# Performance work log

Hardware: AMD Instinct MI355X
Metric: run time of the kernel (lower is better)

The kernel has to match this reference:

```python
import jax, jax.numpy as jnp
import numpy as np

N = 8192
IN_F = 128
N_HID = 64
OUT_F = 128
NEG = -9.0e15


def _xavier(key, shape, gain=1.414):
    fan_in, fan_out = shape
    a = gain * np.sqrt(6.0 / (fan_in + fan_out))
    return jax.random.uniform(key, shape, jnp.float32, -a, a)


def setup_inputs() -> dict:
    key = jax.random.key(0)
    k_h, k_adj, k_ws, k_wt, k_wc = jax.random.split(key, 5)
    h = jax.random.normal(k_h, (N, IN_F), dtype=jnp.float32)
    adj = jax.random.randint(k_adj, (N, N), 0, 2, dtype=jnp.int32)
    Ws = _xavier(k_ws, (IN_F, N_HID))
    Wt = _xavier(k_wt, (IN_F, N_HID))
    Wc = _xavier(k_wc, (IN_F, OUT_F))
    return {"h": h, "adj": adj, "Ws": Ws, "Wt": Wt, "Wc": Wc}


def reference(h, adj, Ws, Wt, Wc):
    # Whs: [N, H], Wht: [N, H]
    Whs = h @ Ws
    Wht = h @ Wt
    # e: [N, N] dense attention scores
    e = jnp.einsum("nh,mh->nm", Whs, Wht)
    z = jnp.where(adj > 0, e, jnp.asarray(NEG, e.dtype))
    alpha = jax.nn.softmax(z, axis=-1)  # [N, N]
    Whc = h @ Wc                        # [N, OUT_F]
    h_prime = alpha @ Whc               # [N, OUT_F]
    return h_prime
```

## Files before the change

### kernel.cpp

```cpp
#include <hip/hip_runtime.h>


#define NN 8192
#define INF_ 128
#define NHID 64
#define OUTF 128
#define NEGC -9.0e15f

typedef unsigned short u16;
typedef __attribute__((ext_vector_type(8))) short bf16x8;
typedef __attribute__((ext_vector_type(4))) float f32x4;
typedef __attribute__((ext_vector_type(4))) int i32x4;
typedef __attribute__((ext_vector_type(4))) unsigned u32x4;

static __device__ __forceinline__ u16 f2bf(float x) {
  union { float f; unsigned u; } v; v.f = x;
  unsigned lsb = (v.u >> 16) & 1u;
  v.u += 0x7fffu + lsb;
  return (u16)(v.u >> 16);
}
static __device__ __forceinline__ float bf2f(u16 h) {
  union { float f; unsigned u; } v; v.u = ((unsigned)h) << 16;
  return v.f;
}
static __device__ __forceinline__ f32x4 mfma16(bf16x8 a, bf16x8 b, f32x4 c) {
  return __builtin_amdgcn_mfma_f32_16x16x32_bf16(a, b, c, 0, 0, 0);
}

__global__ __launch_bounds__(256) void proj_kernel(
    const float* __restrict__ h, const float* __restrict__ Ws,
    const float* __restrict__ Wt, const float* __restrict__ Wc,
    u16* __restrict__ whs_hi, u16* __restrict__ whs_lo,
    u16* __restrict__ wht_hi, u16* __restrict__ wht_lo,
    u16* __restrict__ whcT) {
  __shared__ f32x4 hbuf[8][32];
  const int tid = threadIdx.x;
  const int r0 = blockIdx.x * 8;
  hbuf[tid >> 5][tid & 31] =
      reinterpret_cast<const f32x4*>(h)[(size_t)r0 * 32 + tid];
  __syncthreads();

  float acc[8];
#pragma unroll
  for (int r = 0; r < 8; ++r) acc[r] = 0.f;

  if (tid < 128) {
    const float* W = (tid < 64) ? (Ws + tid) : (Wt + (tid - 64));
#pragma unroll 4
    for (int k4 = 0; k4 < 32; ++k4) {
      float w0 = W[(k4 * 4 + 0) * NHID];
      float w1 = W[(k4 * 4 + 1) * NHID];
      float w2 = W[(k4 * 4 + 2) * NHID];
      float w3 = W[(k4 * 4 + 3) * NHID];
#pragma unroll
      for (int r = 0; r < 8; ++r) {
        f32x4 hv = hbuf[r][k4];
        acc[r] += hv.x * w0 + hv.y * w1 + hv.z * w2 + hv.w * w3;
      }
    }
    const int col = tid & 63;
    u16* hi = (tid < 64) ? whs_hi : wht_hi;
    u16* lo = (tid < 64) ? whs_lo : wht_lo;
#pragma unroll
    for (int r = 0; r < 8; ++r) {
      float v = acc[r];
      u16 hb = f2bf(v);
      hi[(size_t)(r0 + r) * NHID + col] = hb;
      lo[(size_t)(r0 + r) * NHID + col] = f2bf(v - bf2f(hb));
    }
  } else {
    const int col = tid - 128;
    const float* W = Wc + col;
#pragma unroll 4
    for (int k4 = 0; k4 < 32; ++k4) {
      float w0 = W[(k4 * 4 + 0) * OUTF];
      float w1 = W[(k4 * 4 + 1) * OUTF];
      float w2 = W[(k4 * 4 + 2) * OUTF];
      float w3 = W[(k4 * 4 + 3) * OUTF];
#pragma unroll
      for (int r = 0; r < 8; ++r) {
        f32x4 hv = hbuf[r][k4];
        acc[r] += hv.x * w0 + hv.y * w1 + hv.z * w2 + hv.w * w3;
      }
    }
    union { u16 s[8]; u32x4 v; } pk;
#pragma unroll
    for (int r = 0; r < 8; ++r) pk.s[r] = f2bf(acc[r]);
    *reinterpret_cast<u32x4*>(whcT + (size_t)col * NN + r0) = pk.v;
  }
}

__global__ __launch_bounds__(256, 2) void attn_kernel(
    const u16* __restrict__ whs_hi, const u16* __restrict__ whs_lo,
    const u16* __restrict__ wht_hi, const u16* __restrict__ wht_lo,
    const u16* __restrict__ whcT, const int* __restrict__ adj,
    float* __restrict__ Opart, float* __restrict__ mpart,
    float* __restrict__ lpart, float* __restrict__ out,
    int iters, int cshift, int final_write) {
  __shared__ __align__(16) u16 Bst[2][2][64 * 72];
  __shared__ __align__(16) u16 Wst[2][128 * 64];
  __shared__ __align__(16) u16 Pbuf[4][16][72];
  __shared__ __align__(16) u16 Mbuf[2][64][4];

  const int tid = threadIdx.x;
  const int w = tid >> 6;
  const int lane = tid & 63;
  const int q = lane >> 4;
  const int ln = lane & 15;
  const int chunk = blockIdx.x & ((1 << cshift) - 1);
  const int rb = blockIdx.x >> cshift;
  const int rowB = rb * 64;
  const int row0 = rowB + w * 16;

  const int bcol = tid >> 2;
  const int bsh = (tid >> 1) & 1;
  const int bkh = tid & 1;
  const u16* bg = (bsh ? wht_lo : wht_hi) + (size_t)bcol * NHID + bkh * 32;
  const int wocol = tid >> 1;
  const int wjh = tid & 1;
  const u16* wg = whcT + (size_t)wocol * NN + wjh * 32;
  const int wsw0 = ((2 * wjh + 0) ^ (wocol & 3)) * 16;
  const int wsw1 = ((2 * wjh + 1) ^ (wocol & 3)) * 16;
  const int arow = tid >> 2;
  const int agrp = tid & 3;
  const int* ag = adj + (size_t)(rowB + arow) * NN + agrp * 16;

  bf16x8 a_hi[2], a_lo[2];
#pragma unroll
  for (int kh = 0; kh < 2; ++kh) {
    a_hi[kh] = *reinterpret_cast<const bf16x8*>(
        whs_hi + (size_t)(row0 + ln) * NHID + kh * 32 + q * 8);
    a_lo[kh] = *reinterpret_cast<const bf16x8*>(
        whs_lo + (size_t)(row0 + ln) * NHID + kh * 32 + q * 8);
  }

  f32x4 oacc[8];
#pragma unroll
  for (int ot = 0; ot < 8; ++ot)
#pragma unroll
    for (int g = 0; g < 4; ++g) oacc[ot][g] = 0.f;

  float m_old[4], l_run[4];
#pragma unroll
  for (int g = 0; g < 4; ++g) { m_old[g] = -__builtin_inff(); l_run[g] = 0.f; }

  const int jbase = chunk * iters;

  {
    const size_t j0 = (size_t)jbase * 64;
    const u32x4* p = reinterpret_cast<const u32x4*>(bg + j0 * NHID);
    u32x4 b0 = p[0], b1 = p[1], b2 = p[2], b3 = p[3];
    const u32x4* pw = reinterpret_cast<const u32x4*>(wg + j0);
    u32x4 w0 = pw[0], w1 = pw[1], w2 = pw[2], w3 = pw[3];
    const i32x4* pa = reinterpret_cast<const i32x4*>(ag + j0);
    i32x4 a0 = __builtin_nontemporal_load(pa + 0);
    i32x4 a1 = __builtin_nontemporal_load(pa + 1);
    i32x4 a2 = __builtin_nontemporal_load(pa + 2);
    i32x4 a3 = __builtin_nontemporal_load(pa + 3);
    u32x4* d = reinterpret_cast<u32x4*>(&Bst[0][bsh][bcol * 72 + bkh * 32]);
    d[0] = b0; d[1] = b1; d[2] = b2; d[3] = b3;
    u32x4* e0 = reinterpret_cast<u32x4*>(&Wst[0][wocol * 64 + wsw0]);
    e0[0] = w0; e0[1] = w1;
    u32x4* e1 = reinterpret_cast<u32x4*>(&Wst[0][wocol * 64 + wsw1]);
    e1[0] = w2; e1[1] = w3;
    unsigned mw = 0;
    mw |= (a0.x>0?1u:0u)<<0  | (a0.y>0?1u:0u)<<1  | (a0.z>0?1u:0u)<<2  | (a0.w>0?1u:0u)<<3;
    mw |= (a1.x>0?1u:0u)<<4  | (a1.y>0?1u:0u)<<5  | (a1.z>0?1u:0u)<<6  | (a1.w>0?1u:0u)<<7;
    mw |= (a2.x>0?1u:0u)<<8  | (a2.y>0?1u:0u)<<9  | (a2.z>0?1u:0u)<<10 | (a2.w>0?1u:0u)<<11;
    mw |= (a3.x>0?1u:0u)<<12 | (a3.y>0?1u:0u)<<13 | (a3.z>0?1u:0u)<<14 | (a3.w>0?1u:0u)<<15;
    Mbuf[0][arow][agrp] = (u16)mw;
  }
  __syncthreads();

  for (int jt = 0; jt < iters; ++jt) {
    const int buf = jt & 1;

    u32x4 sb0, sb1, sb2, sb3, sw0, sw1, sw2, sw3;
    i32x4 ad0, ad1, ad2, ad3;
    if (jt + 1 < iters) {
      const size_t j1 = (size_t)(jbase + jt + 1) * 64;
      const u32x4* p = reinterpret_cast<const u32x4*>(bg + j1 * NHID);
      sb0 = p[0]; sb1 = p[1]; sb2 = p[2]; sb3 = p[3];
      const u32x4* pw = reinterpret_cast<const u32x4*>(wg + j1);
      sw0 = pw[0]; sw1 = pw[1]; sw2 = pw[2]; sw3 = pw[3];
      const i32x4* pa = reinterpret_cast<const i32x4*>(ag + j1);
      ad0 = __builtin_nontemporal_load(pa + 0);
      ad1 = __builtin_nontemporal_load(pa + 1);
      ad2 = __builtin_nontemporal_load(pa + 2);
      ad3 = __builtin_nontemporal_load(pa + 3);
    }

    unsigned mk01[4], mk23[4];
#pragma unroll
    for (int g = 0; g < 4; ++g) {
      const unsigned* mrow = reinterpret_cast<const unsigned*>(
          &Mbuf[buf][w * 16 + q * 4 + g][0]);
      mk01[g] = mrow[0];
      mk23[g] = mrow[1];
    }

    const u16* Bh = &Bst[buf][0][0];
    const u16* Bl = &Bst[buf][1][0];
    float s[4][4];
#pragma unroll
    for (int nt = 0; nt < 4; ++nt) {
      const int base = (nt * 16 + ln) * 72 + q * 8;
      bf16x8 bh0 = *reinterpret_cast<const bf16x8*>(&Bh[base]);
      bf16x8 bh1 = *reinterpret_cast<const bf16x8*>(&Bh[base + 32]);
      bf16x8 bl0 = *reinterpret_cast<const bf16x8*>(&Bl[base]);
      bf16x8 bl1 = *reinterpret_cast<const bf16x8*>(&Bl[base + 32]);
      f32x4 sa;
#pragma unroll
      for (int g = 0; g < 4; ++g) sa[g] = 0.f;
      sa = mfma16(a_lo[0], bh0, sa);
      sa = mfma16(a_hi[0], bl0, sa);
      sa = mfma16(a_hi[0], bh0, sa);
      sa = mfma16(a_lo[1], bh1, sa);
      sa = mfma16(a_hi[1], bl1, sa);
      sa = mfma16(a_hi[1], bh1, sa);
#pragma unroll
      for (int g = 0; g < 4; ++g) {
        unsigned wrd = (nt == 0) ? (mk01[g] & 0xffffu)
                     : (nt == 1) ? (mk01[g] >> 16)
                     : (nt == 2) ? (mk23[g] & 0xffffu)
                                 : (mk23[g] >> 16);
        s[nt][g] = ((wrd >> ln) & 1u) ? sa[g] : NEGC;
      }
    }

    float mr[4];
#pragma unroll
    for (int g = 0; g < 4; ++g)
      mr[g] = fmaxf(fmaxf(s[0][g], s[1][g]), fmaxf(s[2][g], s[3][g]));
#pragma unroll
    for (int msk = 1; msk <= 8; msk <<= 1)
#pragma unroll
      for (int g = 0; g < 4; ++g) mr[g] = fmaxf(mr[g], __shfl_xor(mr[g], msk));

    float mn[4], alpha[4], ps[4];
#pragma unroll
    for (int g = 0; g < 4; ++g) {
      mn[g] = fmaxf(m_old[g], mr[g]);
      alpha[g] = __expf(m_old[g] - mn[g]);
      m_old[g] = mn[g];
      ps[g] = 0.f;
    }
#pragma unroll
    for (int nt = 0; nt < 4; ++nt)
#pragma unroll
      for (int g = 0; g < 4; ++g) {
        float p = __expf(s[nt][g] - mn[g]);
        ps[g] += p;
        Pbuf[w][q * 4 + g][nt * 16 + ln] = f2bf(p);
      }
#pragma unroll
    for (int msk = 1; msk <= 8; msk <<= 1)
#pragma unroll
      for (int g = 0; g < 4; ++g) ps[g] += __shfl_xor(ps[g], msk);
#pragma unroll
    for (int g = 0; g < 4; ++g) l_run[g] = l_run[g] * alpha[g] + ps[g];
#pragma unroll
    for (int ot = 0; ot < 8; ++ot)
#pragma unroll
      for (int g = 0; g < 4; ++g) oacc[ot][g] *= alpha[g];

#pragma unroll
    for (int kh = 0; kh < 2; ++kh) {
      bf16x8 pa = *reinterpret_cast<const bf16x8*>(
          &Pbuf[w][ln][kh * 32 + q * 8]);
      const int c = kh * 2 + (q >> 1);
      const int sub = (q & 1) * 8;
#pragma unroll
      for (int ot = 0; ot < 8; ++ot) {
        const int ocol = ot * 16 + ln;
        bf16x8 wb = *reinterpret_cast<const bf16x8*>(
            &Wst[buf][ocol * 64 + ((c ^ (ocol & 3)) << 4) + sub]);
        oacc[ot] = mfma16(pa, wb, oacc[ot]);
      }
    }

    if (jt + 1 < iters) {
      const int nb = buf ^ 1;
      u32x4* d = reinterpret_cast<u32x4*>(&Bst[nb][bsh][bcol * 72 + bkh * 32]);
      d[0] = sb0; d[1] = sb1; d[2] = sb2; d[3] = sb3;
      u32x4* e0 = reinterpret_cast<u32x4*>(&Wst[nb][wocol * 64 + wsw0]);
      e0[0] = sw0; e0[1] = sw1;
      u32x4* e1 = reinterpret_cast<u32x4*>(&Wst[nb][wocol * 64 + wsw1]);
      e1[0] = sw2; e1[1] = sw3;
      unsigned mw = 0;
      mw |= (ad0.x>0?1u:0u)<<0  | (ad0.y>0?1u:0u)<<1  | (ad0.z>0?1u:0u)<<2  | (ad0.w>0?1u:0u)<<3;
      mw |= (ad1.x>0?1u:0u)<<4  | (ad1.y>0?1u:0u)<<5  | (ad1.z>0?1u:0u)<<6  | (ad1.w>0?1u:0u)<<7;
      mw |= (ad2.x>0?1u:0u)<<8  | (ad2.y>0?1u:0u)<<9  | (ad2.z>0?1u:0u)<<10 | (ad2.w>0?1u:0u)<<11;
      mw |= (ad3.x>0?1u:0u)<<12 | (ad3.y>0?1u:0u)<<13 | (ad3.z>0?1u:0u)<<14 | (ad3.w>0?1u:0u)<<15;
      Mbuf[buf ^ 1][arow][agrp] = (u16)mw;
    }
    __syncthreads();
  }

  if (final_write) {
#pragma unroll
    for (int ot = 0; ot < 8; ++ot)
#pragma unroll
      for (int g = 0; g < 4; ++g) {
        const int r = row0 + q * 4 + g;
        out[(size_t)r * OUTF + ot * 16 + ln] = oacc[ot][g] / l_run[g];
      }
  } else {
#pragma unroll
    for (int ot = 0; ot < 8; ++ot)
#pragma unroll
      for (int g = 0; g < 4; ++g) {
        const int r = row0 + q * 4 + g;
        Opart[((size_t)chunk * NN + r) * OUTF + ot * 16 + ln] = oacc[ot][g];
      }
    if (ln == 0) {
#pragma unroll
      for (int g = 0; g < 4; ++g) {
        const int r = row0 + q * 4 + g;
        mpart[chunk * NN + r] = m_old[g];
        lpart[chunk * NN + r] = l_run[g];
      }
    }
  }
}

__global__ __launch_bounds__(256) void combine_kernel(
    const float* __restrict__ Opart, const float* __restrict__ mpart,
    const float* __restrict__ lpart, float* __restrict__ out, int C) {
  const int idx = blockIdx.x * 256 + threadIdx.x;
  const int row = idx >> 7;
  float M = -__builtin_inff();
  for (int c = 0; c < C; ++c) M = fmaxf(M, mpart[c * NN + row]);
  float den = 0.f, num = 0.f;
  for (int c = 0; c < C; ++c) {
    float wgt = __expf(mpart[c * NN + row] - M);
    den += lpart[c * NN + row] * wgt;
    num += Opart[(size_t)c * NN * OUTF + idx] * wgt;
  }
  out[idx] = num / den;
}

extern "C" void kernel_launch(void* const* d_in, const int* in_sizes, int n_in,
                              void* d_out, int out_size, void* d_ws, size_t ws_size,
                              hipStream_t stream) {
  const float* h   = (const float*)d_in[0];
  const int*   adj = (const int*)d_in[1];
  const float* Ws  = (const float*)d_in[2];
  const float* Wt  = (const float*)d_in[3];
  const float* Wc  = (const float*)d_in[4];
  float* out = (float*)d_out;

  char* ws = (char*)d_ws;
  const size_t MB = 1024 * 1024;
  u16* whs_hi = (u16*)(ws);
  u16* whs_lo = (u16*)(ws + 1 * MB);
  u16* wht_hi = (u16*)(ws + 2 * MB);
  u16* wht_lo = (u16*)(ws + 3 * MB);
  u16* whcT   = (u16*)(ws + 4 * MB);
  float* mpart = (float*)(ws + 6 * MB);
  float* lpart = (float*)(ws + 6 * MB + 256 * 1024);
  float* Opart = (float*)(ws + 6 * MB + 512 * 1024);

  int C = 4, cshift = 2;
  if (6 * MB + 512 * 1024 + (size_t)C * NN * OUTF * sizeof(float) > ws_size) {
    C = 1; cshift = 0;
  }
  const int final_write = (C == 1) ? 1 : 0;
  const int iters = NN / (C * 64);

  proj_kernel<<<NN / 8, 256, 0, stream>>>(h, Ws, Wt, Wc, whs_hi, whs_lo,
                                          wht_hi, wht_lo, whcT);
  attn_kernel<<<(NN / 64) * C, 256, 0, stream>>>(
      whs_hi, whs_lo, wht_hi, wht_lo, whcT, adj, Opart, mpart, lpart, out,
      iters, cshift, final_write);
  if (!final_write)
    combine_kernel<<<NN * OUTF / 256, 256, 0, stream>>>(Opart, mpart, lpart,
                                                        out, C);
}
```

Measured before the change: 452.9 us.

## Transpose score MFMA, fold log2e into Whs, skip rescale when max unchanged

```diff
diff --git a/kernel.cpp b/kernel.cpp
--- a/kernel.cpp
+++ b/kernel.cpp
@@ -59,11 +59,12 @@
       }
     }
     const int col = tid & 63;
+    const float sc = (tid < 64) ? 1.4426950408889634f : 1.0f;
     u16* hi = (tid < 64) ? whs_hi : wht_hi;
     u16* lo = (tid < 64) ? whs_lo : wht_lo;
 #pragma unroll
     for (int r = 0; r < 8; ++r) {
-      float v = acc[r];
+      float v = acc[r] * sc;
       u16 hb = f2bf(v);
       hi[(size_t)(r0 + r) * NHID + col] = hb;
       lo[(size_t)(r0 + r) * NHID + col] = f2bf(v - bf2f(hb));
@@ -140,9 +141,8 @@
 #pragma unroll
     for (int g = 0; g < 4; ++g) oacc[ot][g] = 0.f;
 
-  float m_old[4], l_run[4];
-#pragma unroll
-  for (int g = 0; g < 4; ++g) { m_old[g] = -__builtin_inff(); l_run[g] = 0.f; }
+  float m_old = -__builtin_inff();
+  float l_run = 0.f;
 
   const int jbase = chunk * iters;
 
@@ -190,14 +190,10 @@
       ad3 = __builtin_nontemporal_load(pa + 3);
     }
 
-    unsigned mk01[4], mk23[4];
-#pragma unroll
-    for (int g = 0; g < 4; ++g) {
-      const unsigned* mrow = reinterpret_cast<const unsigned*>(
-          &Mbuf[buf][w * 16 + q * 4 + g][0]);
-      mk01[g] = mrow[0];
-      mk23[g] = mrow[1];
-    }
+    const unsigned* mrow =
+        reinterpret_cast<const unsigned*>(&Mbuf[buf][w * 16 + ln][0]);
+    const unsigned m0 = mrow[0];
+    const unsigned m1 = mrow[1];
 
     const u16* Bh = &Bst[buf][0][0];
     const u16* Bl = &Bst[buf][1][0];
@@ -212,57 +208,62 @@
       f32x4 sa;
 #pragma unroll
       for (int g = 0; g < 4; ++g) sa[g] = 0.f;
-      sa = mfma16(a_lo[0], bh0, sa);
-      sa = mfma16(a_hi[0], bl0, sa);
-      sa = mfma16(a_hi[0], bh0, sa);
-      sa = mfma16(a_lo[1], bh1, sa);
-      sa = mfma16(a_hi[1], bl1, sa);
-      sa = mfma16(a_hi[1], bh1, sa);
+      sa = mfma16(bh0, a_lo[0], sa);
+      sa = mfma16(bl0, a_hi[0], sa);
+      sa = mfma16(bh0, a_hi[0], sa);
+      sa = mfma16(bh1, a_lo[1], sa);
+      sa = mfma16(bl1, a_hi[1], sa);
+      sa = mfma16(bh1, a_hi[1], sa);
+      const unsigned mm = (nt & 2) ? m1 : m0;
 #pragma unroll
       for (int g = 0; g < 4; ++g) {
-        unsigned wrd = (nt == 0) ? (mk01[g] & 0xffffu)
-                     : (nt == 1) ? (mk01[g] >> 16)
-                     : (nt == 2) ? (mk23[g] & 0xffffu)
-                                 : (mk23[g] >> 16);
-        s[nt][g] = ((wrd >> ln) & 1u) ? sa[g] : NEGC;
-      }
-    }
-
-    float mr[4];
-#pragma unroll
-    for (int g = 0; g < 4; ++g)
-      mr[g] = fmaxf(fmaxf(s[0][g], s[1][g]), fmaxf(s[2][g], s[3][g]));
-#pragma unroll
-    for (int msk = 1; msk <= 8; msk <<= 1)
-#pragma unroll
-      for (int g = 0; g < 4; ++g) mr[g] = fmaxf(mr[g], __shfl_xor(mr[g], msk));
-
-    float mn[4], alpha[4], ps[4];
-#pragma unroll
-    for (int g = 0; g < 4; ++g) {
-      mn[g] = fmaxf(m_old[g], mr[g]);
-      alpha[g] = __expf(m_old[g] - mn[g]);
-      m_old[g] = mn[g];
-      ps[g] = 0.f;
-    }
-#pragma unroll
-    for (int nt = 0; nt < 4; ++nt)
-#pragma unroll
-      for (int g = 0; g < 4; ++g) {
-        float p = __expf(s[nt][g] - mn[g]);
-        ps[g] += p;
-        Pbuf[w][q * 4 + g][nt * 16 + ln] = f2bf(p);
-      }
-#pragma unroll
-    for (int msk = 1; msk <= 8; msk <<= 1)
-#pragma unroll
-      for (int g = 0; g < 4; ++g) ps[g] += __shfl_xor(ps[g], msk);
-#pragma unroll
-    for (int g = 0; g < 4; ++g) l_run[g] = l_run[g] * alpha[g] + ps[g];
-#pragma unroll
-    for (int ot = 0; ot < 8; ++ot)
-#pragma unroll
-      for (int g = 0; g < 4; ++g) oacc[ot][g] *= alpha[g];
+        unsigned bit = (mm >> ((nt & 1) * 16 + q * 4 + g)) & 1u;
+        s[nt][g] = bit ? sa[g] : NEGC;
+      }
+    }
+
+    float rmax;
+    {
+      float t0 = fmaxf(fmaxf(s[0][0], s[0][1]), fmaxf(s[0][2], s[0][3]));
+      float t1 = fmaxf(fmaxf(s[1][0], s[1][1]), fmaxf(s[1][2], s[1][3]));
+      float t2 = fmaxf(fmaxf(s[2][0], s[2][1]), fmaxf(s[2][2], s[2][3]));
+      float t3 = fmaxf(fmaxf(s[3][0], s[3][1]), fmaxf(s[3][2], s[3][3]));
+      rmax = fmaxf(fmaxf(t0, t1), fmaxf(t2, t3));
+    }
+    rmax = fmaxf(rmax, __shfl_xor(rmax, 16));
+    rmax = fmaxf(rmax, __shfl_xor(rmax, 32));
+
+    if (__any(rmax > m_old)) {
+      const float mn = fmaxf(m_old, rmax);
+      const float al = __builtin_amdgcn_exp2f(m_old - mn);
+      m_old = mn;
+      l_run *= al;
+      float alg[4];
+#pragma unroll
+      for (int g = 0; g < 4; ++g) alg[g] = __shfl(al, q * 4 + g);
+#pragma unroll
+      for (int ot = 0; ot < 8; ++ot)
+#pragma unroll
+        for (int g = 0; g < 4; ++g) oacc[ot][g] *= alg[g];
+    }
+
+    float ps = 0.f;
+#pragma unroll
+    for (int nt = 0; nt < 4; ++nt) {
+      float p0 = __builtin_amdgcn_exp2f(s[nt][0] - m_old);
+      float p1 = __builtin_amdgcn_exp2f(s[nt][1] - m_old);
+      float p2 = __builtin_amdgcn_exp2f(s[nt][2] - m_old);
+      float p3 = __builtin_amdgcn_exp2f(s[nt][3] - m_old);
+      ps += (p0 + p1) + (p2 + p3);
+      union { u16 h[4]; unsigned long long u; } pk;
+      pk.h[0] = f2bf(p0); pk.h[1] = f2bf(p1);
+      pk.h[2] = f2bf(p2); pk.h[3] = f2bf(p3);
+      *reinterpret_cast<unsigned long long*>(
+          &Pbuf[w][ln][nt * 16 + q * 4]) = pk.u;
+    }
+    ps += __shfl_xor(ps, 16);
+    ps += __shfl_xor(ps, 32);
+    l_run += ps;
 
 #pragma unroll
     for (int kh = 0; kh < 2; ++kh) {
@@ -298,12 +299,15 @@
   }
 
   if (final_write) {
+    float lr[4];
+#pragma unroll
+    for (int g = 0; g < 4; ++g) lr[g] = __shfl(l_run, q * 4 + g);
 #pragma unroll
     for (int ot = 0; ot < 8; ++ot)
 #pragma unroll
       for (int g = 0; g < 4; ++g) {
         const int r = row0 + q * 4 + g;
-        out[(size_t)r * OUTF + ot * 16 + ln] = oacc[ot][g] / l_run[g];
+        out[(size_t)r * OUTF + ot * 16 + ln] = oacc[ot][g] / lr[g];
       }
   } else {
 #pragma unroll
@@ -313,13 +317,9 @@
         const int r = row0 + q * 4 + g;
         Opart[((size_t)chunk * NN + r) * OUTF + ot * 16 + ln] = oacc[ot][g];
       }
-    if (ln == 0) {
-#pragma unroll
-      for (int g = 0; g < 4; ++g) {
-        const int r = row0 + q * 4 + g;
-        mpart[chunk * NN + r] = m_old[g];
-        lpart[chunk * NN + r] = l_run[g];
-      }
+    if (lane < 16) {
+      mpart[chunk * NN + row0 + ln] = m_old;
+      lpart[chunk * NN + row0 + ln] = l_run;
     }
   }
 }
@@ -333,7 +333,7 @@
   for (int c = 0; c < C; ++c) M = fmaxf(M, mpart[c * NN + row]);
   float den = 0.f, num = 0.f;
   for (int c = 0; c < C; ++c) {
-    float wgt = __expf(mpart[c * NN + row] - M);
+    float wgt = __builtin_amdgcn_exp2f(mpart[c * NN + row] - M);
     den += lpart[c * NN + row] * wgt;
     num += Opart[(size_t)c * NN * OUTF + idx] * wgt;
   }
```

New measurement: 439.0 us. 3.1% less time.
